# Kernel optimization log

Measured on AMD Instinct MI355X. Metric: run time of the kernel, lower is better.

Reference implementation:

```python
import jax, jax.numpy as jnp
from jax import lax
import numpy as np

WIN = 8          # window side -> N = 64 tokens per window
DIM = 256
HEADS = 8
B_ = 4096        # batch * num_windows
DN = ('NCHW', 'OIHW', 'NCHW')


def _rel_pos_index(win):
    ch = np.arange(win)
    coords = np.stack(np.meshgrid(ch, ch, indexing='ij'))
    flat = coords.reshape(2, -1)
    rel = flat[:, :, None] - flat[:, None, :]                      # [2,N,N]
    rel = rel.transpose(1, 2, 0).astype(np.int32)                  # [N,N,2]
    rel[..., 0] += win - 1
    rel[..., 1] += win - 1
    rel[..., 0] *= 2 * win - 1
    return rel.sum(-1)                                             # [N,N] in [0, (2w-1)^2)


def _sepconv(x, dw_w, dw_b, pw_w, pw_b):
    # x: [B,C,H,W]; depthwise 3x3 (groups=C) + bias + ReLU, then pointwise 1x1 + bias
    C = x.shape[1]
    y = lax.conv_general_dilated(x, dw_w, (1, 1), [(1, 1), (1, 1)],
                                 dimension_numbers=DN, feature_group_count=C)
    y = jax.nn.relu(y + dw_b[None, :, None, None])
    y = lax.conv_general_dilated(y, pw_w, (1, 1), [(0, 0), (0, 0)],
                                 dimension_numbers=DN)
    return y + pw_b[None, :, None, None]


def setup_inputs() -> dict:
    key = jax.random.key(0)
    ks = jax.random.split(key, 16)
    C = DIM
    d = {}
    d['x'] = jax.random.normal(ks[0], (B_, WIN * WIN, C), dtype=jnp.float32)
    for i, p in enumerate(['q', 'k', 'v']):
        d[f'{p}_dw_w'] = jax.random.normal(ks[1 + 4 * i], (C, 1, 3, 3), jnp.float32) * 0.05
        d[f'{p}_dw_b'] = jax.random.normal(ks[2 + 4 * i], (C,), jnp.float32) * 0.02
        d[f'{p}_pw_w'] = jax.random.normal(ks[3 + 4 * i], (C, C, 1, 1), jnp.float32) * 0.05
        d[f'{p}_pw_b'] = jax.random.normal(ks[4 + 4 * i], (C,), jnp.float32) * 0.02
    d['bias_table'] = jax.random.normal(ks[13], ((2 * WIN - 1) ** 2, HEADS), jnp.float32) * 0.02
    d['proj_w'] = jax.random.normal(ks[14], (C, C), jnp.float32) * 0.02
    d['proj_b'] = jax.random.normal(ks[15], (C,), jnp.float32) * 0.02
    d['rel_index'] = jnp.asarray(_rel_pos_index(WIN))  # [N,N] int32
    return d


def reference(x, q_dw_w, q_dw_b, q_pw_w, q_pw_b,
              k_dw_w, k_dw_b, k_pw_w, k_pw_b,
              v_dw_w, v_dw_b, v_pw_w, v_pw_b,
              bias_table, proj_w, proj_b, rel_index):
    B, N, C = x.shape
    H = HEADS
    dh = C // H
    scale = dh ** (-0.5)
    l = WIN
    xi = x.transpose(0, 2, 1).reshape(B, C, l, l)          # b (l w) c -> b c l w
    q = _sepconv(xi, q_dw_w, q_dw_b, q_pw_w, q_pw_b)
    k = _sepconv(xi, k_dw_w, k_dw_b, k_pw_w, k_pw_b)
    v = _sepconv(xi, v_dw_w, v_dw_b, v_pw_w, v_pw_b)
    # b (h d) l w -> b h (l w) d
    q = q.reshape(B, H, dh, N).transpose(0, 1, 3, 2)
    k = k.reshape(B, H, dh, N).transpose(0, 1, 3, 2)
    v = v.reshape(B, H, dh, N).transpose(0, 1, 3, 2)
    attn = jnp.einsum('bhnd,bhmd->bhnm', q * scale, k)     # [B,H,N,N]
    bias = bias_table[rel_index]                           # [N,N,H] gather
    attn = attn + bias.transpose(2, 0, 1)[None]            # ratio=1, repeat is identity
    attn = jax.nn.softmax(attn, axis=-1)
    out = jnp.einsum('bhnm,bhmd->bhnd', attn, v)           # [B,H,N,dh]
    out = out.transpose(0, 2, 1, 3).reshape(B, N, C)
    return out @ proj_w.T + proj_b
```

## Files before the change

### kernel.cpp

```cpp
#include <hip/hip_runtime.h>

typedef __attribute__((ext_vector_type(8))) short bf16x8;
typedef __attribute__((ext_vector_type(4))) float f32x4;

#define XK_B 0
#define S_B  32768
#define Q_B  49152
#define K1_S 32768
#define K2_P 32768

#define QWS_SHORTS 67108864ull

__device__ __forceinline__ unsigned short f2b(float f) {
  unsigned int v = __builtin_bit_cast(unsigned int, f);
  v += 0x7FFFu + ((v >> 16) & 1u);
  return (unsigned short)(v >> 16);
}
__device__ __forceinline__ unsigned int pk2(float a, float b) {
  return (unsigned int)f2b(a) | ((unsigned int)f2b(b) << 16);
}
__device__ __forceinline__ bf16x8 pack8(const float4& a, const float4& b) {
  union { unsigned int u[4]; bf16x8 v; } x;
  x.u[0] = pk2(a.x, a.y); x.u[1] = pk2(a.z, a.w);
  x.u[2] = pk2(b.x, b.y); x.u[3] = pk2(b.z, b.w);
  return x.v;
}
__device__ __forceinline__ float lo16(unsigned int u) { return __builtin_bit_cast(float, u << 16); }
__device__ __forceinline__ float hi16(unsigned int u) { return __builtin_bit_cast(float, u & 0xFFFF0000u); }

__global__ void transpose_dw_kernel(const float* __restrict__ w0,
                                    const float* __restrict__ w1,
                                    const float* __restrict__ w2,
                                    float* __restrict__ out) {
  int i = blockIdx.x * 256 + threadIdx.x;
  if (i >= 6912) return;
  int p = i / 2304, r = i % 2304, tap = r >> 8, c = r & 255;
  const float* w = (p == 0) ? w0 : ((p == 1) ? w1 : w2);
  out[i] = w[c * 9 + tap];
}

__global__ __launch_bounds__(512, 2) void qkv_kernel(
    const float* __restrict__ xg,
    const float* __restrict__ dwb0, const float* __restrict__ pww0, const float* __restrict__ pwb0,
    const float* __restrict__ dwb1, const float* __restrict__ pww1, const float* __restrict__ pwb1,
    const float* __restrict__ dwb2, const float* __restrict__ pww2, const float* __restrict__ pwb2,
    const float* __restrict__ dwT,
    unsigned short* __restrict__ qkv)
{
  __shared__ __align__(16) unsigned char smem[49152];
  const int tid  = threadIdx.x;
  const int lane = tid & 63;
  const int wv   = tid >> 6;
  const int lc   = lane & 15;
  const int lq2  = lane >> 4;
  const int b    = blockIdx.x;
  const float* xb = xg + (size_t)b * 16384;
  const f32x4 zero4 = {0.f, 0.f, 0.f, 0.f};

#pragma unroll
  for (int it = 0; it < 4; ++it) {
    const int g   = tid + it * 512;
    const int n   = g >> 5;
    const int c16 = g & 31;
    const float4 wa = *(const float4*)(xb + n * 256 + c16 * 8);
    const float4 wb = *(const float4*)(xb + n * 256 + c16 * 8 + 4);
    *(bf16x8*)(smem + XK_B + n * 512 + ((c16 ^ (n & 7))) * 16) = pack8(wa, wb);
  }
  __syncthreads();

  auto dwconv = [&](int s, const float* __restrict__ dwb, const float* __restrict__ dT) {
    const int c4    = tid & 31;
    const int strip = tid >> 5;
    const int l   = strip >> 1;
    const int w0c = (strip & 1) * 4;
    const int cb  = s * 128 + c4 * 4;
    const int c16 = s * 16 + (c4 >> 1);
    const int hb8 = (c4 & 1) * 8;
    float o[4][4];
    {
      const f32x4 bv = *(const f32x4*)(dwb + cb);
#pragma unroll
      for (int t = 0; t < 4; ++t)
#pragma unroll
        for (int j = 0; j < 4; ++j) o[t][j] = bv[j];
    }
#pragma unroll
    for (int dl = 0; dl < 3; ++dl) {
      const int row = l + dl - 1;
      const bool rok = (row >= 0) && (row < 8);
      float wt[3][4];
#pragma unroll
      for (int dc = 0; dc < 3; ++dc) {
        const f32x4 wv0 = *(const f32x4*)(dT + (dl * 3 + dc) * 256 + cb);
#pragma unroll
        for (int j = 0; j < 4; ++j) wt[dc][j] = wv0[j];
      }
#pragma unroll
      for (int jc = 0; jc < 6; ++jc) {
        const int col = w0c + jc - 1;
        float xc[4];
        if (rok && col >= 0 && col < 8) {
          const int t = row * 8 + col;
          const uint2 u = *(const uint2*)(smem + XK_B + t * 512 + ((c16 ^ (t & 7))) * 16 + hb8);
          xc[0] = lo16(u.x); xc[1] = hi16(u.x);
          xc[2] = lo16(u.y); xc[3] = hi16(u.y);
        } else {
#pragma unroll
          for (int j = 0; j < 4; ++j) xc[j] = 0.f;
        }
#pragma unroll
        for (int dc = 0; dc < 3; ++dc) {
          const int ot = jc - dc;
          if (ot >= 0 && ot < 4) {
#pragma unroll
            for (int j = 0; j < 4; ++j) o[ot][j] = fmaf(wt[dc][j], xc[j], o[ot][j]);
          }
        }
      }
    }
#pragma unroll
    for (int t = 0; t < 4; ++t) {
      const int n = l * 8 + w0c + t;
      uint2 u;
      u.x = pk2(fmaxf(o[t][0], 0.f), fmaxf(o[t][1], 0.f));
      u.y = pk2(fmaxf(o[t][2], 0.f), fmaxf(o[t][3], 0.f));
      *(uint2*)(smem + K1_S + n * 256 + (((c4 >> 1) ^ (n & 15)) & 15) * 16 + hb8) = u;
    }
  };

#pragma unroll 1
  for (int qk = 0; qk < 2; ++qk) {
    const float* W   = qk ? pww1 : pww0;
    const float* pwb = qk ? pwb1 : pwb0;
    const float* dwb = qk ? dwb1 : dwb0;
    const float* dT  = dwT + qk * 2304;
    f32x4 acc[2][4];
#pragma unroll
    for (int cot = 0; cot < 2; ++cot)
#pragma unroll
      for (int nt = 0; nt < 4; ++nt) acc[cot][nt] = zero4;

#pragma unroll 1
    for (int s = 0; s < 2; ++s) {
      dwconv(s, dwb, dT);
      __syncthreads();
#pragma unroll
      for (int kk = 0; kk < 4; ++kk) {
        bf16x8 afrW[2];
#pragma unroll
        for (int cot = 0; cot < 2; ++cot) {
          const int co = 32 * wv + 16 * cot + lc;
          const int ci0 = s * 128 + 32 * kk + 8 * lq2;
          const float4 wa = *(const float4*)(W + co * 256 + ci0);
          const float4 wb = *(const float4*)(W + co * 256 + ci0 + 4);
          afrW[cot] = pack8(wa, wb);
        }
        bf16x8 bfr[4];
#pragma unroll
        for (int nt = 0; nt < 4; ++nt) {
          const int n = 16 * nt + lc;
          bfr[nt] = *(const bf16x8*)(smem + K1_S + n * 256 + (((4 * kk + lq2) ^ (n & 15)) & 15) * 16);
        }
#pragma unroll
        for (int cot = 0; cot < 2; ++cot)
#pragma unroll
          for (int nt = 0; nt < 4; ++nt)
            acc[cot][nt] = __builtin_amdgcn_mfma_f32_16x16x32_bf16(afrW[cot], bfr[nt], acc[cot][nt], 0, 0, 0);
      }
      __syncthreads();
    }
    unsigned short* dst = qkv + (qk ? QWS_SHORTS : 0) + ((size_t)(b * 8 + wv) * 4) * 512;
    unsigned char* Sb = smem + K1_S + wv * 2048;
#pragma unroll
    for (int rr = 0; rr < 2; ++rr) {
#pragma unroll
      for (int cot = 0; cot < 2; ++cot) {
        const int c0 = 32 * wv + 16 * cot + 4 * lq2;
        const f32x4 pb = *(const f32x4*)(pwb + c0);
        const int o8 = 2 * cot + (lq2 >> 1);
#pragma unroll
        for (int nt2 = 0; nt2 < 2; ++nt2) {
          const int nt = 2 * rr + nt2;
          const int nn = 16 * nt2 + lc;
          uint2 u;
          u.x = pk2(acc[cot][nt][0] + pb[0], acc[cot][nt][1] + pb[1]);
          u.y = pk2(acc[cot][nt][2] + pb[2], acc[cot][nt][3] + pb[3]);
          *(uint2*)(Sb + nn * 64 + ((o8 ^ (nn & 3)) * 16) + (lq2 & 1) * 8) = u;
        }
      }
#pragma unroll
      for (int mtl = 0; mtl < 2; ++mtl) {
        const int nn = 16 * mtl + lc;
        const bf16x8 fr = *(const bf16x8*)(Sb + nn * 64 + ((lq2 ^ (nn & 3)) * 16));
        *(bf16x8*)(dst + (2 * rr + mtl) * 512 + lane * 8) = fr;
      }
    }
    __syncthreads();
  }

  {
    f32x4 av[4][2];
#pragma unroll
    for (int i = 0; i < 4; ++i)
#pragma unroll
      for (int t = 0; t < 2; ++t) av[i][t] = zero4;

#pragma unroll 1
    for (int s = 0; s < 2; ++s) {
      dwconv(s, dwb2, dwT + 2 * 2304);
      __syncthreads();
#pragma unroll
      for (int kk = 0; kk < 4; ++kk) {
        bf16x8 afr[4];
#pragma unroll
        for (int i = 0; i < 4; ++i) {
          const int m = 16 * i + lc;
          afr[i] = *(const bf16x8*)(smem + K1_S + m * 256 + (((4 * kk + lq2) ^ (m & 15)) & 15) * 16);
        }
        bf16x8 bb[2];
#pragma unroll
        for (int t = 0; t < 2; ++t) {
          const int co = 16 * (2 * wv + t) + lc;
          const int ci0 = s * 128 + 32 * kk + 8 * lq2;
          const float4 wa = *(const float4*)(pww2 + co * 256 + ci0);
          const float4 wb = *(const float4*)(pww2 + co * 256 + ci0 + 4);
          bb[t] = pack8(wa, wb);
        }
#pragma unroll
        for (int i = 0; i < 4; ++i)
#pragma unroll
          for (int t = 0; t < 2; ++t)
            av[i][t] = __builtin_amdgcn_mfma_f32_16x16x32_bf16(afr[i], bb[t], av[i][t], 0, 0, 0);
      }
      __syncthreads();
    }
    unsigned short* dst = qkv + 2 * QWS_SHORTS + ((size_t)(b * 8 + wv) * 4) * 512;
#pragma unroll
    for (int t = 0; t < 2; ++t) {
      const float pb = pwb2[16 * (2 * wv + t) + lc];
#pragma unroll
      for (int i = 0; i < 4; ++i) {
        const int m0 = 16 * i + 4 * lq2;
        uint2 u;
        u.x = pk2(av[i][t][0] + pb, av[i][t][1] + pb);
        u.y = pk2(av[i][t][2] + pb, av[i][t][3] + pb);
        *(uint2*)(smem + K1_S + wv * 2048 + lc * 128 +
                  (((m0 >> 3) ^ (lc & 7)) & 7) * 16 + (lq2 & 1) * 8) = u;
      }
#pragma unroll
      for (int kk = 0; kk < 2; ++kk) {
        const bf16x8 vf = *(const bf16x8*)(smem + K1_S + wv * 2048 + lc * 128 +
                                           (((4 * kk + lq2) ^ (lc & 7)) & 7) * 16);
        *(bf16x8*)(dst + (t * 2 + kk) * 512 + lane * 8) = vf;
      }
    }
  }
}

__global__ __launch_bounds__(512, 2) void attnproj_kernel(
    const unsigned short* __restrict__ qkv,
    const float* __restrict__ bt,
    const float* __restrict__ pjw, const float* __restrict__ pjb,
    const int* __restrict__ rel,
    float* __restrict__ outg)
{
  __shared__ __align__(16) unsigned char smem[49152];
  const int tid  = threadIdx.x;
  const int lane = tid & 63;
  const int wv   = tid >> 6;
  const int lc   = lane & 15;
  const int lq2  = lane >> 4;
  const int b    = blockIdx.x;
  const f32x4 zero4 = {0.f, 0.f, 0.f, 0.f};

  const unsigned short* qw = qkv + ((size_t)(b * 8 + wv) * 4) * 512;
  const unsigned short* kw = qw + QWS_SHORTS;
  const unsigned short* vw = qw + 2 * QWS_SHORTS;

  bf16x8 kfrag[4];
#pragma unroll
  for (int mt = 0; mt < 4; ++mt)
    kfrag[mt] = *(const bf16x8*)(kw + mt * 512 + lane * 8);
  bf16x8 vfrag[2][2];
#pragma unroll
  for (int t = 0; t < 2; ++t)
#pragma unroll
    for (int kk = 0; kk < 2; ++kk)
      vfrag[t][kk] = *(const bf16x8*)(vw + (t * 2 + kk) * 512 + lane * 8);

  const float scale = 0.17677669529663687f;
  const int h = wv;
#pragma unroll
  for (int qt = 0; qt < 4; ++qt) {
    const int n = 16 * qt + lc;
    const bf16x8 qfrag = *(const bf16x8*)(qw + qt * 512 + lane * 8);
    f32x4 sc[4];
#pragma unroll
    for (int mt = 0; mt < 4; ++mt)
      sc[mt] = __builtin_amdgcn_mfma_f32_16x16x32_bf16(kfrag[mt], qfrag, zero4, 0, 0, 0);
    const int* relrow = rel + n * 64;
    float sv[4][4];
#pragma unroll
    for (int mt = 0; mt < 4; ++mt)
#pragma unroll
      for (int r = 0; r < 4; ++r) {
        const int m = 16 * mt + 4 * lq2 + r;
        sv[mt][r] = sc[mt][r] * scale + bt[relrow[m] * 8 + h];
      }
    float mx = sv[0][0];
#pragma unroll
    for (int mt = 0; mt < 4; ++mt)
#pragma unroll
      for (int r = 0; r < 4; ++r) mx = fmaxf(mx, sv[mt][r]);
    mx = fmaxf(mx, __shfl_xor(mx, 16));
    mx = fmaxf(mx, __shfl_xor(mx, 32));
    float sum = 0.f;
#pragma unroll
    for (int mt = 0; mt < 4; ++mt)
#pragma unroll
      for (int r = 0; r < 4; ++r) {
        sv[mt][r] = __expf(sv[mt][r] - mx);
        sum += sv[mt][r];
      }
    sum += __shfl_xor(sum, 16);
    sum += __shfl_xor(sum, 32);
    const float rinv = __builtin_amdgcn_rcpf(sum);
#pragma unroll
    for (int mt = 0; mt < 4; ++mt) {
      const int m0 = 16 * mt + 4 * lq2;
      uint2 u;
      u.x = pk2(sv[mt][0], sv[mt][1]);
      u.y = pk2(sv[mt][2], sv[mt][3]);
      *(uint2*)(smem + K2_P + wv * 2048 + lc * 128 +
                (((m0 >> 3) ^ (lc & 7)) & 7) * 16 + (lq2 & 1) * 8) = u;
    }
    f32x4 o[2] = {zero4, zero4};
#pragma unroll
    for (int kk = 0; kk < 2; ++kk) {
      const bf16x8 pf = *(const bf16x8*)(smem + K2_P + wv * 2048 + lc * 128 +
                                         (((4 * kk + lq2) ^ (lc & 7)) & 7) * 16);
#pragma unroll
      for (int ct = 0; ct < 2; ++ct)
        o[ct] = __builtin_amdgcn_mfma_f32_16x16x32_bf16(vfrag[ct][kk], pf, o[ct], 0, 0, 0);
    }
#pragma unroll
    for (int ct = 0; ct < 2; ++ct) {
      const int c0 = 32 * h + 16 * ct + 4 * lq2;
      uint2 u;
      u.x = pk2(o[ct][0] * rinv, o[ct][1] * rinv);
      u.y = pk2(o[ct][2] * rinv, o[ct][3] * rinv);
      *(uint2*)(smem + n * 512 + (((c0 >> 3) ^ (n & 31)) & 31) * 16 + (lq2 & 1) * 8) = u;
    }
  }
  __syncthreads();

  {
    f32x4 pacc[4][2];
#pragma unroll
    for (int i = 0; i < 4; ++i)
#pragma unroll
      for (int t = 0; t < 2; ++t) pacc[i][t] = zero4;
#pragma unroll
    for (int kk = 0; kk < 8; ++kk) {
      bf16x8 afr[4];
#pragma unroll
      for (int i = 0; i < 4; ++i) {
        const int n = 16 * i + lc;
        afr[i] = *(const bf16x8*)(smem + n * 512 + (((4 * kk + lq2) ^ (n & 31)) & 31) * 16);
      }
      bf16x8 bb[2];
#pragma unroll
      for (int t = 0; t < 2; ++t) {
        const int co = 16 * (2 * wv + t) + lc;
        const float4 wa = *(const float4*)(pjw + co * 256 + 32 * kk + 8 * lq2);
        const float4 wb = *(const float4*)(pjw + co * 256 + 32 * kk + 8 * lq2 + 4);
        bb[t] = pack8(wa, wb);
      }
#pragma unroll
      for (int i = 0; i < 4; ++i)
#pragma unroll
        for (int t = 0; t < 2; ++t)
          pacc[i][t] = __builtin_amdgcn_mfma_f32_16x16x32_bf16(afr[i], bb[t], pacc[i][t], 0, 0, 0);
    }
    float* og = outg + (size_t)b * 16384;
#pragma unroll
    for (int t = 0; t < 2; ++t) {
      const int co = 16 * (2 * wv + t) + lc;
      const float pbv = pjb[co];
#pragma unroll
      for (int i = 0; i < 4; ++i)
#pragma unroll
        for (int r = 0; r < 4; ++r)
          og[(16 * i + 4 * lq2 + r) * 256 + co] = pacc[i][t][r] + pbv;
    }
  }
}

template<int USE_WS>
__global__ __launch_bounds__(512, 2) void winattn_kernel(
    const float* __restrict__ xg,
    const float* __restrict__ dww0, const float* __restrict__ dwb0,
    const float* __restrict__ pww0, const float* __restrict__ pwb0,
    const float* __restrict__ dww1, const float* __restrict__ dwb1,
    const float* __restrict__ pww1, const float* __restrict__ pwb1,
    const float* __restrict__ dww2, const float* __restrict__ dwb2,
    const float* __restrict__ pww2, const float* __restrict__ pwb2,
    const float* __restrict__ bt,
    const float* __restrict__ pjw, const float* __restrict__ pjb,
    const int* __restrict__ rel,
    const float* __restrict__ wsT,
    float* __restrict__ outg)
{
  __shared__ __align__(16) unsigned char smem[81920];
  const int tid  = threadIdx.x;
  const int lane = tid & 63;
  const int wv   = tid >> 6;
  const int lc   = lane & 15;
  const int lq2  = lane >> 4;
  const int b    = blockIdx.x;
  const float* xb = xg + (size_t)b * 16384;
  const f32x4 zero4 = {0.f, 0.f, 0.f, 0.f};

#pragma unroll
  for (int it = 0; it < 4; ++it) {
    const int g   = tid + it * 512;
    const int n   = g >> 5;
    const int c16 = g & 31;
    const float4 wa = *(const float4*)(xb + n * 256 + c16 * 8);
    const float4 wb = *(const float4*)(xb + n * 256 + c16 * 8 + 4);
    *(bf16x8*)(smem + XK_B + n * 512 + ((c16 ^ (n & 7))) * 16) = pack8(wa, wb);
  }
  __syncthreads();

  auto dwconv = [&](int s, const float* __restrict__ dwb,
                    const float* __restrict__ dwwT, const float* __restrict__ dwwR) {
    const int c4    = tid & 31;
    const int strip = tid >> 5;
    const int l   = strip >> 1;
    const int w0c = (strip & 1) * 4;
    const int cb  = s * 128 + c4 * 4;
    const int c16 = s * 16 + (c4 >> 1);
    const int hb8 = (c4 & 1) * 8;
    float o[4][4];
    {
      const f32x4 bv = *(const f32x4*)(dwb + cb);
#pragma unroll
      for (int t = 0; t < 4; ++t)
#pragma unroll
        for (int j = 0; j < 4; ++j) o[t][j] = bv[j];
    }
#pragma unroll
    for (int dl = 0; dl < 3; ++dl) {
      const int row = l + dl - 1;
      const bool rok = (row >= 0) && (row < 8);
      float wt[3][4];
#pragma unroll
      for (int dc = 0; dc < 3; ++dc) {
        if (USE_WS) {
          const f32x4 wv0 = *(const f32x4*)(dwwT + (dl * 3 + dc) * 256 + cb);
#pragma unroll
          for (int j = 0; j < 4; ++j) wt[dc][j] = wv0[j];
        } else {
#pragma unroll
          for (int j = 0; j < 4; ++j) wt[dc][j] = dwwR[(cb + j) * 9 + dl * 3 + dc];
        }
      }
#pragma unroll
      for (int jc = 0; jc < 6; ++jc) {
        const int col = w0c + jc - 1;
        float xc[4];
        if (rok && col >= 0 && col < 8) {
          const int t = row * 8 + col;
          const uint2 u = *(const uint2*)(smem + XK_B + t * 512 + ((c16 ^ (t & 7))) * 16 + hb8);
          xc[0] = lo16(u.x); xc[1] = hi16(u.x);
          xc[2] = lo16(u.y); xc[3] = hi16(u.y);
        } else {
#pragma unroll
          for (int j = 0; j < 4; ++j) xc[j] = 0.f;
        }
#pragma unroll
        for (int dc = 0; dc < 3; ++dc) {
          const int ot = jc - dc;
          if (ot >= 0 && ot < 4) {
#pragma unroll
            for (int j = 0; j < 4; ++j) o[ot][j] = fmaf(wt[dc][j], xc[j], o[ot][j]);
          }
        }
      }
    }
#pragma unroll
    for (int t = 0; t < 4; ++t) {
      const int n = l * 8 + w0c + t;
      uint2 u;
      u.x = pk2(fmaxf(o[t][0], 0.f), fmaxf(o[t][1], 0.f));
      u.y = pk2(fmaxf(o[t][2], 0.f), fmaxf(o[t][3], 0.f));
      *(uint2*)(smem + S_B + n * 256 + (((c4 >> 1) ^ (n & 15)) & 15) * 16 + hb8) = u;
    }
  };

  bf16x8 vfrag[2][2];
  {
    f32x4 av[4][2];
#pragma unroll
    for (int i = 0; i < 4; ++i)
#pragma unroll
      for (int t = 0; t < 2; ++t) av[i][t] = zero4;
#pragma unroll 1
    for (int s = 0; s < 2; ++s) {
      dwconv(s, dwb2, USE_WS ? (wsT + 2 * 2304) : nullptr, dww2);
      __syncthreads();
#pragma unroll
      for (int kk = 0; kk < 4; ++kk) {
        bf16x8 afr[4];
#pragma unroll
        for (int i = 0; i < 4; ++i) {
          const int m = 16 * i + lc;
          afr[i] = *(const bf16x8*)(smem + S_B + m * 256 + (((4 * kk + lq2) ^ (m & 15)) & 15) * 16);
        }
        bf16x8 bb[2];
#pragma unroll
        for (int t = 0; t < 2; ++t) {
          const int co = 16 * (2 * wv + t) + lc;
          const int ci0 = s * 128 + 32 * kk + 8 * lq2;
          const float4 wa = *(const float4*)(pww2 + co * 256 + ci0);
          const float4 wb = *(const float4*)(pww2 + co * 256 + ci0 + 4);
          bb[t] = pack8(wa, wb);
        }
#pragma unroll
        for (int i = 0; i < 4; ++i)
#pragma unroll
          for (int t = 0; t < 2; ++t)
            av[i][t] = __builtin_amdgcn_mfma_f32_16x16x32_bf16(afr[i], bb[t], av[i][t], 0, 0, 0);
      }
      __syncthreads();
    }
#pragma unroll
    for (int t = 0; t < 2; ++t) {
      const float pb = pwb2[16 * (2 * wv + t) + lc];
#pragma unroll
      for (int i = 0; i < 4; ++i) {
        const int m0 = 16 * i + 4 * lq2;
        uint2 u;
        u.x = pk2(av[i][t][0] + pb, av[i][t][1] + pb);
        u.y = pk2(av[i][t][2] + pb, av[i][t][3] + pb);
        *(uint2*)(smem + S_B + wv * 2048 + lc * 128 +
                  (((m0 >> 3) ^ (lc & 7)) & 7) * 16 + (lq2 & 1) * 8) = u;
      }
#pragma unroll
      for (int kk = 0; kk < 2; ++kk)
        vfrag[t][kk] = *(const bf16x8*)(smem + S_B + wv * 2048 + lc * 128 +
                                        (((4 * kk + lq2) ^ (lc & 7)) & 7) * 16);
    }
  }
  __syncthreads();

#pragma unroll 1
  for (int qk = 0; qk < 2; ++qk) {
    const int dstB = qk ? XK_B : Q_B;
    const float* W   = qk ? pww1 : pww0;
    const float* pwb = qk ? pwb1 : pwb0;
    const float* dwb = qk ? dwb1 : dwb0;
    const float* dwT = USE_WS ? (wsT + qk * 2304) : nullptr;
    const float* dwR = qk ? dww1 : dww0;
    f32x4 acc[2][4];
#pragma unroll
    for (int cot = 0; cot < 2; ++cot)
#pragma unroll
      for (int nt = 0; nt < 4; ++nt) acc[cot][nt] = zero4;
#pragma unroll 1
    for (int s = 0; s < 2; ++s) {
      dwconv(s, dwb, dwT, dwR);
      __syncthreads();
#pragma unroll
      for (int kk = 0; kk < 4; ++kk) {
        bf16x8 afrW[2];
#pragma unroll
        for (int cot = 0; cot < 2; ++cot) {
          const int co = 32 * wv + 16 * cot + lc;
          const int ci0 = s * 128 + 32 * kk + 8 * lq2;
          const float4 wa = *(const float4*)(W + co * 256 + ci0);
          const float4 wb = *(const float4*)(W + co * 256 + ci0 + 4);
          afrW[cot] = pack8(wa, wb);
        }
        bf16x8 bfr[4];
#pragma unroll
        for (int nt = 0; nt < 4; ++nt) {
          const int n = 16 * nt + lc;
          bfr[nt] = *(const bf16x8*)(smem + S_B + n * 256 + (((4 * kk + lq2) ^ (n & 15)) & 15) * 16);
        }
#pragma unroll
        for (int cot = 0; cot < 2; ++cot)
#pragma unroll
          for (int nt = 0; nt < 4; ++nt)
            acc[cot][nt] = __builtin_amdgcn_mfma_f32_16x16x32_bf16(afrW[cot], bfr[nt], acc[cot][nt], 0, 0, 0);
      }
      __syncthreads();
    }
#pragma unroll
    for (int cot = 0; cot < 2; ++cot) {
      const int c0 = 32 * wv + 16 * cot + 4 * lq2;
      const f32x4 pb = *(const f32x4*)(pwb + c0);
#pragma unroll
      for (int nt = 0; nt < 4; ++nt) {
        const int n = 16 * nt + lc;
        uint2 u;
        u.x = pk2(acc[cot][nt][0] + pb[0], acc[cot][nt][1] + pb[1]);
        u.y = pk2(acc[cot][nt][2] + pb[2], acc[cot][nt][3] + pb[3]);
        *(uint2*)(smem + dstB + n * 512 + (((c0 >> 3) ^ (n & 31)) & 31) * 16 + (lq2 & 1) * 8) = u;
      }
    }
  }

  {
    const int h = wv;
    bf16x8 kfrag[4];
#pragma unroll
    for (int mt = 0; mt < 4; ++mt) {
      const int m = 16 * mt + lc;
      kfrag[mt] = *(const bf16x8*)(smem + XK_B + m * 512 + (((4 * h + lq2) ^ (m & 31)) & 31) * 16);
    }
    const float scale = 0.17677669529663687f;
#pragma unroll
    for (int qt = 0; qt < 4; ++qt) {
      const int n = 16 * qt + lc;
      const bf16x8 qfrag = *(const bf16x8*)(smem + Q_B + n * 512 + (((4 * h + lq2) ^ (n & 31)) & 31) * 16);
      f32x4 sc[4];
#pragma unroll
      for (int mt = 0; mt < 4; ++mt)
        sc[mt] = __builtin_amdgcn_mfma_f32_16x16x32_bf16(kfrag[mt], qfrag, zero4, 0, 0, 0);
      const int* relrow = rel + n * 64;
      float sv[4][4];
#pragma unroll
      for (int mt = 0; mt < 4; ++mt)
#pragma unroll
        for (int r = 0; r < 4; ++r) {
          const int m = 16 * mt + 4 * lq2 + r;
          sv[mt][r] = sc[mt][r] * scale + bt[relrow[m] * 8 + h];
        }
      float mx = sv[0][0];
#pragma unroll
      for (int mt = 0; mt < 4; ++mt)
#pragma unroll
        for (int r = 0; r < 4; ++r) mx = fmaxf(mx, sv[mt][r]);
      mx = fmaxf(mx, __shfl_xor(mx, 16));
      mx = fmaxf(mx, __shfl_xor(mx, 32));
      float sum = 0.f;
#pragma unroll
      for (int mt = 0; mt < 4; ++mt)
#pragma unroll
        for (int r = 0; r < 4; ++r) {
          sv[mt][r] = __expf(sv[mt][r] - mx);
          sum += sv[mt][r];
        }
      sum += __shfl_xor(sum, 16);
      sum += __shfl_xor(sum, 32);
      const float rinv = __builtin_amdgcn_rcpf(sum);
#pragma unroll
      for (int mt = 0; mt < 4; ++mt) {
        const int m0 = 16 * mt + 4 * lq2;
        uint2 u;
        u.x = pk2(sv[mt][0], sv[mt][1]);
        u.y = pk2(sv[mt][2], sv[mt][3]);
        *(uint2*)(smem + S_B + wv * 2048 + lc * 128 +
                  (((m0 >> 3) ^ (lc & 7)) & 7) * 16 + (lq2 & 1) * 8) = u;
      }
      f32x4 o[2] = {zero4, zero4};
#pragma unroll
      for (int kk = 0; kk < 2; ++kk) {
        const bf16x8 pf = *(const bf16x8*)(smem + S_B + wv * 2048 + lc * 128 +
                                           (((4 * kk + lq2) ^ (lc & 7)) & 7) * 16);
#pragma unroll
        for (int ct = 0; ct < 2; ++ct)
          o[ct] = __builtin_amdgcn_mfma_f32_16x16x32_bf16(vfrag[ct][kk], pf, o[ct], 0, 0, 0);
      }
#pragma unroll
      for (int ct = 0; ct < 2; ++ct) {
        const int c0 = 32 * h + 16 * ct + 4 * lq2;
        uint2 u;
        u.x = pk2(o[ct][0] * rinv, o[ct][1] * rinv);
        u.y = pk2(o[ct][2] * rinv, o[ct][3] * rinv);
        *(uint2*)(smem + XK_B + n * 512 + (((c0 >> 3) ^ (n & 31)) & 31) * 16 + (lq2 & 1) * 8) = u;
      }
    }
  }
  __syncthreads();

  {
    f32x4 pacc[4][2];
#pragma unroll
    for (int i = 0; i < 4; ++i)
#pragma unroll
      for (int t = 0; t < 2; ++t) pacc[i][t] = zero4;
#pragma unroll
    for (int kk = 0; kk < 8; ++kk) {
      bf16x8 afr[4];
#pragma unroll
      for (int i = 0; i < 4; ++i) {
        const int n = 16 * i + lc;
        afr[i] = *(const bf16x8*)(smem + XK_B + n * 512 + (((4 * kk + lq2) ^ (n & 31)) & 31) * 16);
      }
      bf16x8 bb[2];
#pragma unroll
      for (int t = 0; t < 2; ++t) {
        const int co = 16 * (2 * wv + t) + lc;
        const float4 wa = *(const float4*)(pjw + co * 256 + 32 * kk + 8 * lq2);
        const float4 wb = *(const float4*)(pjw + co * 256 + 32 * kk + 8 * lq2 + 4);
        bb[t] = pack8(wa, wb);
      }
#pragma unroll
      for (int i = 0; i < 4; ++i)
#pragma unroll
        for (int t = 0; t < 2; ++t)
          pacc[i][t] = __builtin_amdgcn_mfma_f32_16x16x32_bf16(afr[i], bb[t], pacc[i][t], 0, 0, 0);
    }
    float* og = outg + (size_t)b * 16384;
#pragma unroll
    for (int t = 0; t < 2; ++t) {
      const int co = 16 * (2 * wv + t) + lc;
      const float pbv = pjb[co];
#pragma unroll
      for (int i = 0; i < 4; ++i)
#pragma unroll
        for (int r = 0; r < 4; ++r)
          og[(16 * i + 4 * lq2 + r) * 256 + co] = pacc[i][t][r] + pbv;
    }
  }
}

extern "C" void kernel_launch(void* const* d_in, const int* in_sizes, int n_in,
                              void* d_out, int out_size, void* d_ws, size_t ws_size,
                              hipStream_t stream) {
  (void)in_sizes; (void)n_in; (void)out_size;
  const float* x    = (const float*)d_in[0];
  const float* qdww = (const float*)d_in[1];
  const float* qdwb = (const float*)d_in[2];
  const float* qpww = (const float*)d_in[3];
  const float* qpwb = (const float*)d_in[4];
  const float* kdww = (const float*)d_in[5];
  const float* kdwb = (const float*)d_in[6];
  const float* kpww = (const float*)d_in[7];
  const float* kpwb = (const float*)d_in[8];
  const float* vdww = (const float*)d_in[9];
  const float* vdwb = (const float*)d_in[10];
  const float* vpww = (const float*)d_in[11];
  const float* vpwb = (const float*)d_in[12];
  const float* bt   = (const float*)d_in[13];
  const float* pjw  = (const float*)d_in[14];
  const float* pjb  = (const float*)d_in[15];
  const int* rel    = (const int*)d_in[16];
  float* out        = (float*)d_out;

  const size_t SPLIT_WS = 32768ull + 3ull * QWS_SHORTS * 2ull;
  if (ws_size >= SPLIT_WS && d_ws != nullptr) {
    float* wsT = (float*)d_ws;
    unsigned short* qkv = (unsigned short*)((char*)d_ws + 32768);
    hipLaunchKernelGGL(transpose_dw_kernel, dim3(27), dim3(256), 0, stream,
                       qdww, kdww, vdww, wsT);
    hipLaunchKernelGGL(qkv_kernel, dim3(4096), dim3(512), 0, stream,
                       x, qdwb, qpww, qpwb, kdwb, kpww, kpwb, vdwb, vpww, vpwb, wsT, qkv);
    hipLaunchKernelGGL(attnproj_kernel, dim3(4096), dim3(512), 0, stream,
                       qkv, bt, pjw, pjb, rel, out);
  } else if (ws_size >= 27648 && d_ws != nullptr) {
    float* wsT = (float*)d_ws;
    hipLaunchKernelGGL(transpose_dw_kernel, dim3(27), dim3(256), 0, stream,
                       qdww, kdww, vdww, wsT);
    hipLaunchKernelGGL((winattn_kernel<1>), dim3(4096), dim3(512), 0, stream,
                       x, qdww, qdwb, qpww, qpwb, kdww, kdwb, kpww, kpwb,
                       vdww, vdwb, vpww, vpwb, bt, pjw, pjb, rel, wsT, out);
  } else {
    hipLaunchKernelGGL((winattn_kernel<0>), dim3(4096), dim3(512), 0, stream,
                       x, qdww, qdwb, qpww, qpwb, kdww, kdwb, kpww, kpwb,
                       vdww, vdwb, vpww, vpwb, bt, pjw, pjb, rel, (const float*)nullptr, out);
  }
}
```

Before: 986.2 us.

## Restructure qkv and attnproj kernels for higher occupancy with smaller accumulators

Raises launch bounds from 2 to 4 blocks per CU for the qkv and attention/projection kernels. To fit that register budget, the pointwise GEMMs now produce output in halves with smaller accumulator arrays, and K fragments are reloaded per query tile instead of held in registers. The qkv kernel computes both depthwise halves up front into a larger 80KB LDS buffer, so it needs fewer barriers. Risks: the larger LDS footprint may cap occupancy anyway, W/pjw global weight loads are repeated, and register pressure could cause spills.

```diff
diff --git a/kernel.cpp b/kernel.cpp
--- a/kernel.cpp
+++ b/kernel.cpp
@@ -6,7 +6,8 @@
 #define XK_B 0
 #define S_B  32768
 #define Q_B  49152
-#define K1_S 32768
+#define K1_S0 32768
+#define K1_BN 65536
 #define K2_P 32768
 
 #define QWS_SHORTS 67108864ull
@@ -39,7 +40,7 @@
   out[i] = w[c * 9 + tap];
 }
 
-__global__ __launch_bounds__(512, 2) void qkv_kernel(
+__global__ __launch_bounds__(512, 4) void qkv_kernel(
     const float* __restrict__ xg,
     const float* __restrict__ dwb0, const float* __restrict__ pww0, const float* __restrict__ pwb0,
     const float* __restrict__ dwb1, const float* __restrict__ pww1, const float* __restrict__ pwb1,
@@ -47,7 +48,7 @@
     const float* __restrict__ dwT,
     unsigned short* __restrict__ qkv)
 {
-  __shared__ __align__(16) unsigned char smem[49152];
+  __shared__ __align__(16) unsigned char smem[81920];
   const int tid  = threadIdx.x;
   const int lane = tid & 63;
   const int wv   = tid >> 6;
@@ -56,6 +57,7 @@
   const int b    = blockIdx.x;
   const float* xb = xg + (size_t)b * 16384;
   const f32x4 zero4 = {0.f, 0.f, 0.f, 0.f};
+  unsigned char* Sb = smem + K1_BN + wv * 2048;
 
 #pragma unroll
   for (int it = 0; it < 4; ++it) {
@@ -69,6 +71,7 @@
   __syncthreads();
 
   auto dwconv = [&](int s, const float* __restrict__ dwb, const float* __restrict__ dT) {
+    unsigned char* Ss = smem + K1_S0 + s * 16384;
     const int c4    = tid & 31;
     const int strip = tid >> 5;
     const int l   = strip >> 1;
@@ -124,8 +127,13 @@
       uint2 u;
       u.x = pk2(fmaxf(o[t][0], 0.f), fmaxf(o[t][1], 0.f));
       u.y = pk2(fmaxf(o[t][2], 0.f), fmaxf(o[t][3], 0.f));
-      *(uint2*)(smem + K1_S + n * 256 + (((c4 >> 1) ^ (n & 15)) & 15) * 16 + hb8) = u;
-    }
+      *(uint2*)(Ss + n * 256 + (((c4 >> 1) ^ (n & 15)) & 15) * 16 + hb8) = u;
+    }
+  };
+
+  auto sfrag = [&](int m, int kk) -> bf16x8 {
+    return *(const bf16x8*)(smem + K1_S0 + (kk >> 2) * 16384 + m * 256 +
+                            (((4 * (kk & 3) + lq2) ^ (m & 15)) & 15) * 16);
   };
 
 #pragma unroll 1
@@ -134,45 +142,38 @@
     const float* pwb = qk ? pwb1 : pwb0;
     const float* dwb = qk ? dwb1 : dwb0;
     const float* dT  = dwT + qk * 2304;
-    f32x4 acc[2][4];
-#pragma unroll
-    for (int cot = 0; cot < 2; ++cot)
-#pragma unroll
-      for (int nt = 0; nt < 4; ++nt) acc[cot][nt] = zero4;
-
+    dwconv(0, dwb, dT);
+    dwconv(1, dwb, dT);
+    __syncthreads();
+    unsigned short* dst = qkv + (qk ? QWS_SHORTS : 0) + ((size_t)(b * 8 + wv) * 4) * 512;
 #pragma unroll 1
-    for (int s = 0; s < 2; ++s) {
-      dwconv(s, dwb, dT);
-      __syncthreads();
-#pragma unroll
-      for (int kk = 0; kk < 4; ++kk) {
+    for (int rr = 0; rr < 2; ++rr) {
+      f32x4 acc[2][2];
+#pragma unroll
+      for (int cot = 0; cot < 2; ++cot)
+#pragma unroll
+        for (int nt2 = 0; nt2 < 2; ++nt2) acc[cot][nt2] = zero4;
+#pragma unroll
+      for (int kk = 0; kk < 8; ++kk) {
         bf16x8 afrW[2];
 #pragma unroll
         for (int cot = 0; cot < 2; ++cot) {
           const int co = 32 * wv + 16 * cot + lc;
-          const int ci0 = s * 128 + 32 * kk + 8 * lq2;
+          const int ci0 = 32 * kk + 8 * lq2;
           const float4 wa = *(const float4*)(W + co * 256 + ci0);
           const float4 wb = *(const float4*)(W + co * 256 + ci0 + 4);
           afrW[cot] = pack8(wa, wb);
         }
-        bf16x8 bfr[4];
-#pragma unroll
-        for (int nt = 0; nt < 4; ++nt) {
-          const int n = 16 * nt + lc;
-          bfr[nt] = *(const bf16x8*)(smem + K1_S + n * 256 + (((4 * kk + lq2) ^ (n & 15)) & 15) * 16);
-        }
+        bf16x8 bfr[2];
+#pragma unroll
+        for (int nt2 = 0; nt2 < 2; ++nt2)
+          bfr[nt2] = sfrag(16 * (2 * rr + nt2) + lc, kk);
 #pragma unroll
         for (int cot = 0; cot < 2; ++cot)
 #pragma unroll
-          for (int nt = 0; nt < 4; ++nt)
-            acc[cot][nt] = __builtin_amdgcn_mfma_f32_16x16x32_bf16(afrW[cot], bfr[nt], acc[cot][nt], 0, 0, 0);
-      }
-      __syncthreads();
-    }
-    unsigned short* dst = qkv + (qk ? QWS_SHORTS : 0) + ((size_t)(b * 8 + wv) * 4) * 512;
-    unsigned char* Sb = smem + K1_S + wv * 2048;
-#pragma unroll
-    for (int rr = 0; rr < 2; ++rr) {
+          for (int nt2 = 0; nt2 < 2; ++nt2)
+            acc[cot][nt2] = __builtin_amdgcn_mfma_f32_16x16x32_bf16(afrW[cot], bfr[nt2], acc[cot][nt2], 0, 0, 0);
+      }
 #pragma unroll
       for (int cot = 0; cot < 2; ++cot) {
         const int c0 = 32 * wv + 16 * cot + 4 * lq2;
@@ -180,11 +181,10 @@
         const int o8 = 2 * cot + (lq2 >> 1);
 #pragma unroll
         for (int nt2 = 0; nt2 < 2; ++nt2) {
-          const int nt = 2 * rr + nt2;
           const int nn = 16 * nt2 + lc;
           uint2 u;
-          u.x = pk2(acc[cot][nt][0] + pb[0], acc[cot][nt][1] + pb[1]);
-          u.y = pk2(acc[cot][nt][2] + pb[2], acc[cot][nt][3] + pb[3]);
+          u.x = pk2(acc[cot][nt2][0] + pb[0], acc[cot][nt2][1] + pb[1]);
+          u.y = pk2(acc[cot][nt2][2] + pb[2], acc[cot][nt2][3] + pb[3]);
           *(uint2*)(Sb + nn * 64 + ((o8 ^ (nn & 3)) * 16) + (lq2 & 1) * 8) = u;
         }
       }
@@ -199,65 +199,47 @@
   }
 
   {
-    f32x4 av[4][2];
-#pragma unroll
-    for (int i = 0; i < 4; ++i)
-#pragma unroll
-      for (int t = 0; t < 2; ++t) av[i][t] = zero4;
-
+    dwconv(0, dwb2, dwT + 2 * 2304);
+    dwconv(1, dwb2, dwT + 2 * 2304);
+    __syncthreads();
+    unsigned short* dst = qkv + 2 * QWS_SHORTS + ((size_t)(b * 8 + wv) * 4) * 512;
 #pragma unroll 1
-    for (int s = 0; s < 2; ++s) {
-      dwconv(s, dwb2, dwT + 2 * 2304);
-      __syncthreads();
-#pragma unroll
-      for (int kk = 0; kk < 4; ++kk) {
-        bf16x8 afr[4];
+    for (int t = 0; t < 2; ++t) {
+      f32x4 av[4];
+#pragma unroll
+      for (int i = 0; i < 4; ++i) av[i] = zero4;
+#pragma unroll
+      for (int kk = 0; kk < 8; ++kk) {
+        const int co = 16 * (2 * wv + t) + lc;
+        const int ci0 = 32 * kk + 8 * lq2;
+        const float4 wa = *(const float4*)(pww2 + co * 256 + ci0);
+        const float4 wb = *(const float4*)(pww2 + co * 256 + ci0 + 4);
+        const bf16x8 bb = pack8(wa, wb);
 #pragma unroll
         for (int i = 0; i < 4; ++i) {
-          const int m = 16 * i + lc;
-          afr[i] = *(const bf16x8*)(smem + K1_S + m * 256 + (((4 * kk + lq2) ^ (m & 15)) & 15) * 16);
-        }
-        bf16x8 bb[2];
-#pragma unroll
-        for (int t = 0; t < 2; ++t) {
-          const int co = 16 * (2 * wv + t) + lc;
-          const int ci0 = s * 128 + 32 * kk + 8 * lq2;
-          const float4 wa = *(const float4*)(pww2 + co * 256 + ci0);
-          const float4 wb = *(const float4*)(pww2 + co * 256 + ci0 + 4);
-          bb[t] = pack8(wa, wb);
-        }
-#pragma unroll
-        for (int i = 0; i < 4; ++i)
-#pragma unroll
-          for (int t = 0; t < 2; ++t)
-            av[i][t] = __builtin_amdgcn_mfma_f32_16x16x32_bf16(afr[i], bb[t], av[i][t], 0, 0, 0);
-      }
-      __syncthreads();
-    }
-    unsigned short* dst = qkv + 2 * QWS_SHORTS + ((size_t)(b * 8 + wv) * 4) * 512;
-#pragma unroll
-    for (int t = 0; t < 2; ++t) {
+          const bf16x8 afr = sfrag(16 * i + lc, kk);
+          av[i] = __builtin_amdgcn_mfma_f32_16x16x32_bf16(afr, bb, av[i], 0, 0, 0);
+        }
+      }
       const float pb = pwb2[16 * (2 * wv + t) + lc];
 #pragma unroll
       for (int i = 0; i < 4; ++i) {
         const int m0 = 16 * i + 4 * lq2;
         uint2 u;
-        u.x = pk2(av[i][t][0] + pb, av[i][t][1] + pb);
-        u.y = pk2(av[i][t][2] + pb, av[i][t][3] + pb);
-        *(uint2*)(smem + K1_S + wv * 2048 + lc * 128 +
-                  (((m0 >> 3) ^ (lc & 7)) & 7) * 16 + (lq2 & 1) * 8) = u;
-      }
-#pragma unroll
-      for (int kk = 0; kk < 2; ++kk) {
-        const bf16x8 vf = *(const bf16x8*)(smem + K1_S + wv * 2048 + lc * 128 +
-                                           (((4 * kk + lq2) ^ (lc & 7)) & 7) * 16);
-        *(bf16x8*)(dst + (t * 2 + kk) * 512 + lane * 8) = vf;
+        u.x = pk2(av[i][0] + pb, av[i][1] + pb);
+        u.y = pk2(av[i][2] + pb, av[i][3] + pb);
+        *(uint2*)(Sb + lc * 128 + (((m0 >> 3) ^ (lc & 7)) & 7) * 16 + (lq2 & 1) * 8) = u;
+      }
+#pragma unroll
+      for (int kk2 = 0; kk2 < 2; ++kk2) {
+        const bf16x8 vf = *(const bf16x8*)(Sb + lc * 128 + (((4 * kk2 + lq2) ^ (lc & 7)) & 7) * 16);
+        *(bf16x8*)(dst + (t * 2 + kk2) * 512 + lane * 8) = vf;
       }
     }
   }
 }
 
-__global__ __launch_bounds__(512, 2) void attnproj_kernel(
+__global__ __launch_bounds__(512, 4) void attnproj_kernel(
     const unsigned short* __restrict__ qkv,
     const float* __restrict__ bt,
     const float* __restrict__ pjw, const float* __restrict__ pjb,
@@ -277,10 +259,6 @@
   const unsigned short* kw = qw + QWS_SHORTS;
   const unsigned short* vw = qw + 2 * QWS_SHORTS;
 
-  bf16x8 kfrag[4];
-#pragma unroll
-  for (int mt = 0; mt < 4; ++mt)
-    kfrag[mt] = *(const bf16x8*)(kw + mt * 512 + lane * 8);
   bf16x8 vfrag[2][2];
 #pragma unroll
   for (int t = 0; t < 2; ++t)
@@ -290,14 +268,16 @@
 
   const float scale = 0.17677669529663687f;
   const int h = wv;
-#pragma unroll
+#pragma unroll 1
   for (int qt = 0; qt < 4; ++qt) {
     const int n = 16 * qt + lc;
     const bf16x8 qfrag = *(const bf16x8*)(qw + qt * 512 + lane * 8);
     f32x4 sc[4];
 #pragma unroll
-    for (int mt = 0; mt < 4; ++mt)
-      sc[mt] = __builtin_amdgcn_mfma_f32_16x16x32_bf16(kfrag[mt], qfrag, zero4, 0, 0, 0);
+    for (int mt = 0; mt < 4; ++mt) {
+      const bf16x8 kfrag = *(const bf16x8*)(kw + mt * 512 + lane * 8);
+      sc[mt] = __builtin_amdgcn_mfma_f32_16x16x32_bf16(kfrag, qfrag, zero4, 0, 0, 0);
+    }
     const int* relrow = rel + n * 64;
     float sv[4][4];
 #pragma unroll
@@ -354,45 +334,31 @@
   }
   __syncthreads();
 
-  {
-    f32x4 pacc[4][2];
+  float* og = outg + (size_t)b * 16384;
+#pragma unroll 1
+  for (int t = 0; t < 2; ++t) {
+    const int co = 16 * (2 * wv + t) + lc;
+    f32x4 pacc[4];
+#pragma unroll
+    for (int i = 0; i < 4; ++i) pacc[i] = zero4;
+#pragma unroll
+    for (int kk = 0; kk < 8; ++kk) {
+      const float4 wa = *(const float4*)(pjw + co * 256 + 32 * kk + 8 * lq2);
+      const float4 wb = *(const float4*)(pjw + co * 256 + 32 * kk + 8 * lq2 + 4);
+      const bf16x8 bb = pack8(wa, wb);
+#pragma unroll
+      for (int i = 0; i < 4; ++i) {
+        const int nn = 16 * i + lc;
+        const bf16x8 afr = *(const bf16x8*)(smem + nn * 512 + (((4 * kk + lq2) ^ (nn & 31)) & 31) * 16);
+        pacc[i] = __builtin_amdgcn_mfma_f32_16x16x32_bf16(afr, bb, pacc[i], 0, 0, 0);
+      }
+    }
+    const float pbv = pjb[co];
 #pragma unroll
     for (int i = 0; i < 4; ++i)
 #pragma unroll
-      for (int t = 0; t < 2; ++t) pacc[i][t] = zero4;
-#pragma unroll
-    for (int kk = 0; kk < 8; ++kk) {
-      bf16x8 afr[4];
-#pragma unroll
-      for (int i = 0; i < 4; ++i) {
-        const int n = 16 * i + lc;
-        afr[i] = *(const bf16x8*)(smem + n * 512 + (((4 * kk + lq2) ^ (n & 31)) & 31) * 16);
-      }
-      bf16x8 bb[2];
-#pragma unroll
-      for (int t = 0; t < 2; ++t) {
-        const int co = 16 * (2 * wv + t) + lc;
-        const float4 wa = *(const float4*)(pjw + co * 256 + 32 * kk + 8 * lq2);
-        const float4 wb = *(const float4*)(pjw + co * 256 + 32 * kk + 8 * lq2 + 4);
-        bb[t] = pack8(wa, wb);
-      }
-#pragma unroll
-      for (int i = 0; i < 4; ++i)
-#pragma unroll
-        for (int t = 0; t < 2; ++t)
-          pacc[i][t] = __builtin_amdgcn_mfma_f32_16x16x32_bf16(afr[i], bb[t], pacc[i][t], 0, 0, 0);
-    }
-    float* og = outg + (size_t)b * 16384;
-#pragma unroll
-    for (int t = 0; t < 2; ++t) {
-      const int co = 16 * (2 * wv + t) + lc;
-      const float pbv = pjb[co];
-#pragma unroll
-      for (int i = 0; i < 4; ++i)
-#pragma unroll
-        for (int r = 0; r < 4; ++r)
-          og[(16 * i + 4 * lq2 + r) * 256 + co] = pacc[i][t][r] + pbv;
-    }
+      for (int r = 0; r < 4; ++r)
+        og[(16 * i + 4 * lq2 + r) * 256 + co] = pacc[i][r] + pbv;
   }
 }
 
```

Result: slower. 1.367 ms (+38.6%).
